# Kernel tuning notes

Hardware: AMD Instinct MI355X
Metric: run time of the kernel (lower is better)

The kernel has to match this reference:

```python
import jax, jax.numpy as jnp
import numpy as np

TOP_K = 2  # module default top_k


def setup_inputs() -> dict:
    key = jax.random.key(0)
    k1, k2, k3 = jax.random.split(key, 3)
    B, D, E = 4096, 1024, 64  # tokens, input_dim, num_experts
    return {
        "tensor1": jax.random.normal(k1, (B, D), dtype=jnp.float32),
        "tensor2": jax.random.normal(k2, (B, D), dtype=jnp.float32),
        "gate_weight": jax.random.normal(k3, (E, 2 * D), dtype=jnp.float32) * 0.02,
    }


def reference(tensor1, tensor2, gate_weight):
    # x: (B, 2D)
    x = jnp.concatenate((tensor1, tensor2), axis=-1)
    # pairwise L2 distance between each token and each expert vector
    diff = gate_weight[None, :, :] - x[:, None, :]          # (B, E, 2D)
    logits = -jnp.sqrt(jnp.sum(diff * diff, axis=-1))        # (B, E)
    topk_logits, indices = jax.lax.top_k(logits, TOP_K)      # (B, K)
    gating_weights = jax.nn.softmax(topk_logits, axis=-1)    # (B, K)
    rows = jnp.arange(logits.shape[0])[:, None]              # (B, 1)
    sparse_gating = jnp.zeros_like(logits).at[rows, indices].set(gating_weights)
    return sparse_gating
```

## Files before the change

kernel.cpp:

```cpp
#include <hip/hip_runtime.h>
#include <math.h>

#define NTOK 4096
#define NDIM 1024
#define KTOT 2048
#define NEXP 64
#define MT   64
#define KB   64
#define LSTR 72
#define NKC  8
#define NSTG 4

typedef _Float16 half8 __attribute__((ext_vector_type(8)));
typedef _Float16 half4 __attribute__((ext_vector_type(4)));
typedef float    floatx4 __attribute__((ext_vector_type(4)));

#define XSCALE 16.0f
#define WSCALE 1024.0f
#define INVSCALE (1.0f / (16.0f * 1024.0f))

struct h2pair { _Float16 h, l; };
__device__ __forceinline__ h2pair split2(float v) {
    h2pair r;
    r.h = (_Float16)v;
    r.l = (_Float16)(v - (float)r.h);
    return r;
}

__global__ __launch_bounds__(256) void prep_w(const float* __restrict__ W,
                                              _Float16* __restrict__ Whg,
                                              _Float16* __restrict__ Wlg,
                                              float* __restrict__ nrm) {
    const int e = blockIdx.x, t = threadIdx.x;
    const float* row = W + (size_t)e * KTOT + t * 8;
    const float4 a = *reinterpret_cast<const float4*>(row);
    const float4 b = *reinterpret_cast<const float4*>(row + 4);
    float ss = fmaf(a.x, a.x, fmaf(a.y, a.y, fmaf(a.z, a.z, fmaf(a.w, a.w, 0.f))));
    ss = fmaf(b.x, b.x, fmaf(b.y, b.y, fmaf(b.z, b.z, fmaf(b.w, b.w, ss))));

    const h2pair p0 = split2(a.x * WSCALE), p1 = split2(a.y * WSCALE);
    const h2pair p2 = split2(a.z * WSCALE), p3 = split2(a.w * WSCALE);
    const h2pair p4 = split2(b.x * WSCALE), p5 = split2(b.y * WSCALE);
    const h2pair p6 = split2(b.z * WSCALE), p7 = split2(b.w * WSCALE);
    half8 h, l;
    h[0]=p0.h; h[1]=p1.h; h[2]=p2.h; h[3]=p3.h; h[4]=p4.h; h[5]=p5.h; h[6]=p6.h; h[7]=p7.h;
    l[0]=p0.l; l[1]=p1.l; l[2]=p2.l; l[3]=p3.l; l[4]=p4.l; l[5]=p5.l; l[6]=p6.l; l[7]=p7.l;
    *reinterpret_cast<half8*>(Whg + (size_t)e * KTOT + t * 8) = h;
    *reinterpret_cast<half8*>(Wlg + (size_t)e * KTOT + t * 8) = l;

    #pragma unroll
    for (int off = 32; off > 0; off >>= 1) ss += __shfl_down(ss, off, 64);
    __shared__ float red[4];
    const int lane = t & 63, wv = t >> 6;
    if (lane == 0) red[wv] = ss;
    __syncthreads();
    if (t == 0) nrm[e] = (red[0] + red[1]) + (red[2] + red[3]);
}

__global__ __launch_bounds__(256, 3) void gemm_mfma(const float* __restrict__ t1,
                                                    const float* __restrict__ t2,
                                                    const _Float16* __restrict__ Whg,
                                                    const _Float16* __restrict__ Wlg,
                                                    float* __restrict__ Gp,
                                                    float* __restrict__ Cp) {
    __shared__ _Float16 Xh[MT * LSTR], Xl[MT * LSTR];
    __shared__ _Float16 Wh[NEXP * LSTR], Wl[NEXP * LSTR];

    const int tid  = threadIdx.x;
    const int lane = tid & 63;
    const int wv   = tid >> 6;
    const int srow = tid >> 4;
    const int scol = tid & 15;
    const int wrow = tid >> 2;
    const int wseg = tid & 3;
    const int kc   = blockIdx.y;
    const int kbase = kc * (NSTG * KB);
    const int tok0  = blockIdx.x * MT;

    const float* __restrict__ xsrc = (kbase < NDIM)
        ? (t1 + (size_t)tok0 * NDIM + kbase)
        : (t2 + (size_t)tok0 * NDIM + (kbase - NDIM));
    const _Float16* __restrict__ whsrc = Whg + (size_t)wrow * KTOT + kbase + wseg * 16;
    const _Float16* __restrict__ wlsrc = Wlg + (size_t)wrow * KTOT + kbase + wseg * 16;
    _Float16* whdst = Wh + wrow * LSTR + wseg * 16;
    _Float16* wldst = Wl + wrow * LSTR + wseg * 16;

    floatx4 acc[4];
    #pragma unroll
    for (int j = 0; j < 4; ++j) { acc[j][0] = 0.f; acc[j][1] = 0.f; acc[j][2] = 0.f; acc[j][3] = 0.f; }
    float ssx[4] = {0.f, 0.f, 0.f, 0.f};

    const int frow = lane & 15;
    const int fq   = lane >> 4;
    const _Float16* xh_p = Xh + (16 * wv + frow) * LSTR + fq * 8;
    const _Float16* xl_p = Xl + (16 * wv + frow) * LSTR + fq * 8;

    #pragma unroll
    for (int s = 0; s < NSTG; ++s) {
        {
            const half8 wh0 = *reinterpret_cast<const half8*>(whsrc + s * KB);
            const half8 wh1 = *reinterpret_cast<const half8*>(whsrc + s * KB + 8);
            const half8 wl0 = *reinterpret_cast<const half8*>(wlsrc + s * KB);
            const half8 wl1 = *reinterpret_cast<const half8*>(wlsrc + s * KB + 8);
            *reinterpret_cast<half8*>(whdst)     = wh0;
            *reinterpret_cast<half8*>(whdst + 8) = wh1;
            *reinterpret_cast<half8*>(wldst)     = wl0;
            *reinterpret_cast<half8*>(wldst + 8) = wl1;
        }
        #pragma unroll
        for (int i = 0; i < 4; ++i) {
            const int row = srow + 16 * i;
            const float4 xv = *reinterpret_cast<const float4*>(
                xsrc + (size_t)row * NDIM + s * KB + scol * 4);
            ssx[i] = fmaf(xv.x, xv.x, fmaf(xv.y, xv.y, fmaf(xv.z, xv.z, fmaf(xv.w, xv.w, ssx[i]))));
            const h2pair x0 = split2(xv.x * XSCALE), x1 = split2(xv.y * XSCALE);
            const h2pair x2 = split2(xv.z * XSCALE), x3 = split2(xv.w * XSCALE);
            half4 hx, lx;
            hx[0] = x0.h; hx[1] = x1.h; hx[2] = x2.h; hx[3] = x3.h;
            lx[0] = x0.l; lx[1] = x1.l; lx[2] = x2.l; lx[3] = x3.l;
            *reinterpret_cast<half4*>(Xh + row * LSTR + scol * 4) = hx;
            *reinterpret_cast<half4*>(Xl + row * LSTR + scol * 4) = lx;
        }
        __syncthreads();

        #pragma unroll
        for (int ks = 0; ks < 2; ++ks) {
            const int ko = ks * 32;
            const half8 ah = *reinterpret_cast<const half8*>(xh_p + ko);
            const half8 al = *reinterpret_cast<const half8*>(xl_p + ko);
            half8 bh[4], bl[4];
            #pragma unroll
            for (int j = 0; j < 4; ++j) {
                bh[j] = *reinterpret_cast<const half8*>(Wh + (16 * j + frow) * LSTR + fq * 8 + ko);
                bl[j] = *reinterpret_cast<const half8*>(Wl + (16 * j + frow) * LSTR + fq * 8 + ko);
            }
            #pragma unroll
            for (int j = 0; j < 4; ++j)
                acc[j] = __builtin_amdgcn_mfma_f32_16x16x32_f16(ah, bh[j], acc[j], 0, 0, 0);
            #pragma unroll
            for (int j = 0; j < 4; ++j)
                acc[j] = __builtin_amdgcn_mfma_f32_16x16x32_f16(al, bh[j], acc[j], 0, 0, 0);
            #pragma unroll
            for (int j = 0; j < 4; ++j)
                acc[j] = __builtin_amdgcn_mfma_f32_16x16x32_f16(ah, bl[j], acc[j], 0, 0, 0);
        }
        __syncthreads();
    }

    const int m0 = 16 * wv + fq * 4;
    #pragma unroll
    for (int j = 0; j < 4; ++j) {
        #pragma unroll
        for (int i = 0; i < 4; ++i) {
            Gp[((size_t)kc * NTOK + tok0 + m0 + i) * NEXP + 16 * j + frow] = acc[j][i];
        }
    }

    #pragma unroll
    for (int off = 1; off < 16; off <<= 1) {
        #pragma unroll
        for (int i = 0; i < 4; ++i) ssx[i] += __shfl_xor(ssx[i], off, 64);
    }
    if (scol == 0) {
        #pragma unroll
        for (int i = 0; i < 4; ++i)
            Cp[(size_t)kc * NTOK + tok0 + srow + 16 * i] = ssx[i];
    }
}

__global__ __launch_bounds__(256) void finalize(const float* __restrict__ Gp,
                                                const float* __restrict__ Cp,
                                                const float* __restrict__ nrm,
                                                float* __restrict__ out) {
    const int wv = threadIdx.x >> 6, lane = threadIdx.x & 63;
    const int token = blockIdx.x * 4 + wv;

    float gsum = 0.f, csum = 0.f;
    #pragma unroll
    for (int cix = 0; cix < NKC; ++cix) {
        gsum += Gp[((size_t)cix * NTOK + token) * NEXP + lane];
        csum += Cp[(size_t)cix * NTOK + token];
    }
    const float nv = nrm[lane];

    const float S = fmaf(-2.f * INVSCALE, gsum, csum) + nv;
    const float logit = -sqrtf(S);

    float v1 = logit; int i1 = lane;
    #pragma unroll
    for (int off = 32; off > 0; off >>= 1) {
        float ov = __shfl_xor(v1, off, 64);
        int   oi = __shfl_xor(i1, off, 64);
        if (ov > v1 || (ov == v1 && oi < i1)) { v1 = ov; i1 = oi; }
    }
    float v2 = (lane == i1) ? -__builtin_inff() : logit;
    int   i2 = lane;
    #pragma unroll
    for (int off = 32; off > 0; off >>= 1) {
        float ov = __shfl_xor(v2, off, 64);
        int   oi = __shfl_xor(i2, off, 64);
        if (ov > v2 || (ov == v2 && oi < i2)) { v2 = ov; i2 = oi; }
    }
    const float e2  = expf(v2 - v1);
    const float inv = 1.f / (1.f + e2);
    const float o = (lane == i1) ? inv : ((lane == i2) ? e2 * inv : 0.f);
    out[(size_t)token * NEXP + lane] = o;
}

extern "C" void kernel_launch(void* const* d_in, const int* in_sizes, int n_in,
                              void* d_out, int out_size, void* d_ws, size_t ws_size,
                              hipStream_t stream) {
    const float* t1 = (const float*)d_in[0];
    const float* t2 = (const float*)d_in[1];
    const float* W  = (const float*)d_in[2];
    float* out = (float*)d_out;

    char* ws = (char*)d_ws;
    float*    Gp  = (float*)ws;
    float*    Cp  = Gp + (size_t)NKC * NTOK * NEXP;
    float*    nrm = Cp + (size_t)NKC * NTOK;
    _Float16* Whg = (_Float16*)(nrm + NEXP);
    _Float16* Wlg = Whg + (size_t)NEXP * KTOT;

    prep_w<<<NEXP, 256, 0, stream>>>(W, Whg, Wlg, nrm);
    gemm_mfma<<<dim3(NTOK / MT, NKC), 256, 0, stream>>>(t1, t2, Whg, Wlg, Gp, Cp);
    finalize<<<NTOK / 4, 256, 0, stream>>>(Gp, Cp, nrm, out);
}
```

Measured before the change: 88.98 us.

## Drop LDS staging; load MFMA fragments directly from global with fragment-ordered weights

The weight hi/lo halves are now stored in a fragment-interleaved layout (k-group major, expert, 8 halves), so each lane can load its MFMA B operand straight from global memory. The GEMM kernel no longer stages X or W through shared memory and has no barriers. Each wave independently handles 16 tokens by one K chunk and converts X to hi/lo fp16 in registers. This removes LDS traffic and syncs, at the cost of each wave re-reading the weight slice from L2 instead of sharing it across a block, and of less latency hiding between loads and MFMAs.

Measured after the change: 89.96 us. No clear change (+1.1%).

```diff
diff --git a/kernel.cpp b/kernel.cpp
--- a/kernel.cpp
+++ b/kernel.cpp
@@ -5,14 +5,11 @@
 #define NDIM 1024
 #define KTOT 2048
 #define NEXP 64
-#define MT   64
-#define KB   64
-#define LSTR 72
 #define NKC  8
-#define NSTG 4
+#define KCH  (KTOT / NKC)
+#define NSTEP (KCH / 32)
 
 typedef _Float16 half8 __attribute__((ext_vector_type(8)));
-typedef _Float16 half4 __attribute__((ext_vector_type(4)));
 typedef float    floatx4 __attribute__((ext_vector_type(4)));
 
 #define XSCALE 16.0f
@@ -28,8 +25,8 @@
 }
 
 __global__ __launch_bounds__(256) void prep_w(const float* __restrict__ W,
-                                              _Float16* __restrict__ Whg,
-                                              _Float16* __restrict__ Wlg,
+                                              _Float16* __restrict__ WhT,
+                                              _Float16* __restrict__ WlT,
                                               float* __restrict__ nrm) {
     const int e = blockIdx.x, t = threadIdx.x;
     const float* row = W + (size_t)e * KTOT + t * 8;
@@ -45,8 +42,9 @@
     half8 h, l;
     h[0]=p0.h; h[1]=p1.h; h[2]=p2.h; h[3]=p3.h; h[4]=p4.h; h[5]=p5.h; h[6]=p6.h; h[7]=p7.h;
     l[0]=p0.l; l[1]=p1.l; l[2]=p2.l; l[3]=p3.l; l[4]=p4.l; l[5]=p5.l; l[6]=p6.l; l[7]=p7.l;
-    *reinterpret_cast<half8*>(Whg + (size_t)e * KTOT + t * 8) = h;
-    *reinterpret_cast<half8*>(Wlg + (size_t)e * KTOT + t * 8) = l;
+    const size_t idx = ((size_t)t * NEXP + e) * 8;
+    *reinterpret_cast<half8*>(WhT + idx) = h;
+    *reinterpret_cast<half8*>(WlT + idx) = l;
 
     #pragma unroll
     for (int off = 32; off > 0; off >>= 1) ss += __shfl_down(ss, off, 64);
@@ -57,115 +55,75 @@
     if (t == 0) nrm[e] = (red[0] + red[1]) + (red[2] + red[3]);
 }
 
-__global__ __launch_bounds__(256, 3) void gemm_mfma(const float* __restrict__ t1,
-                                                    const float* __restrict__ t2,
-                                                    const _Float16* __restrict__ Whg,
-                                                    const _Float16* __restrict__ Wlg,
-                                                    float* __restrict__ Gp,
-                                                    float* __restrict__ Cp) {
-    __shared__ _Float16 Xh[MT * LSTR], Xl[MT * LSTR];
-    __shared__ _Float16 Wh[NEXP * LSTR], Wl[NEXP * LSTR];
-
+__global__ __launch_bounds__(256) void gemm_frag(const float* __restrict__ t1,
+                                                 const float* __restrict__ t2,
+                                                 const _Float16* __restrict__ WhT,
+                                                 const _Float16* __restrict__ WlT,
+                                                 float* __restrict__ Gp,
+                                                 float* __restrict__ Cp) {
     const int tid  = threadIdx.x;
     const int lane = tid & 63;
-    const int wv   = tid >> 6;
-    const int srow = tid >> 4;
-    const int scol = tid & 15;
-    const int wrow = tid >> 2;
-    const int wseg = tid & 3;
-    const int kc   = blockIdx.y;
-    const int kbase = kc * (NSTG * KB);
-    const int tok0  = blockIdx.x * MT;
+    const int gw   = blockIdx.x * 4 + (tid >> 6);
+    const int tokg = gw >> 3;
+    const int kc   = gw & 7;
+    const int tok0 = tokg * 16;
+    const int kbase = kc * KCH;
+    const int n  = lane & 15;
+    const int fq = lane >> 4;
 
-    const float* __restrict__ xsrc = (kbase < NDIM)
-        ? (t1 + (size_t)tok0 * NDIM + kbase)
-        : (t2 + (size_t)tok0 * NDIM + (kbase - NDIM));
-    const _Float16* __restrict__ whsrc = Whg + (size_t)wrow * KTOT + kbase + wseg * 16;
-    const _Float16* __restrict__ wlsrc = Wlg + (size_t)wrow * KTOT + kbase + wseg * 16;
-    _Float16* whdst = Wh + wrow * LSTR + wseg * 16;
-    _Float16* wldst = Wl + wrow * LSTR + wseg * 16;
+    const float* __restrict__ xb = ((kbase < NDIM)
+        ? (t1 + (size_t)(tok0 + n) * NDIM + kbase)
+        : (t2 + (size_t)(tok0 + n) * NDIM + (kbase - NDIM))) + fq * 8;
+    const _Float16* __restrict__ whb = WhT + ((size_t)(kbase >> 3) + fq) * (NEXP * 8) + n * 8;
+    const _Float16* __restrict__ wlb = WlT + ((size_t)(kbase >> 3) + fq) * (NEXP * 8) + n * 8;
 
     floatx4 acc[4];
     #pragma unroll
-    for (int j = 0; j < 4; ++j) { acc[j][0] = 0.f; acc[j][1] = 0.f; acc[j][2] = 0.f; acc[j][3] = 0.f; }
-    float ssx[4] = {0.f, 0.f, 0.f, 0.f};
-
-    const int frow = lane & 15;
-    const int fq   = lane >> 4;
-    const _Float16* xh_p = Xh + (16 * wv + frow) * LSTR + fq * 8;
-    const _Float16* xl_p = Xl + (16 * wv + frow) * LSTR + fq * 8;
+    for (int j = 0; j < 4; ++j) { acc[j][0]=0.f; acc[j][1]=0.f; acc[j][2]=0.f; acc[j][3]=0.f; }
+    float ssx = 0.f;
 
     #pragma unroll
-    for (int s = 0; s < NSTG; ++s) {
-        {
-            const half8 wh0 = *reinterpret_cast<const half8*>(whsrc + s * KB);
-            const half8 wh1 = *reinterpret_cast<const half8*>(whsrc + s * KB + 8);
-            const half8 wl0 = *reinterpret_cast<const half8*>(wlsrc + s * KB);
-            const half8 wl1 = *reinterpret_cast<const half8*>(wlsrc + s * KB + 8);
-            *reinterpret_cast<half8*>(whdst)     = wh0;
-            *reinterpret_cast<half8*>(whdst + 8) = wh1;
-            *reinterpret_cast<half8*>(wldst)     = wl0;
-            *reinterpret_cast<half8*>(wldst + 8) = wl1;
+    for (int s = 0; s < NSTEP; ++s) {
+        const float4 x0 = *reinterpret_cast<const float4*>(xb + s * 32);
+        const float4 x1 = *reinterpret_cast<const float4*>(xb + s * 32 + 4);
+        half8 bh[4], bl[4];
+        #pragma unroll
+        for (int j = 0; j < 4; ++j) {
+            bh[j] = *reinterpret_cast<const half8*>(whb + (size_t)s * 4 * (NEXP * 8) + j * 128);
+            bl[j] = *reinterpret_cast<const half8*>(wlb + (size_t)s * 4 * (NEXP * 8) + j * 128);
         }
+        ssx = fmaf(x0.x, x0.x, fmaf(x0.y, x0.y, fmaf(x0.z, x0.z, fmaf(x0.w, x0.w, ssx))));
+        ssx = fmaf(x1.x, x1.x, fmaf(x1.y, x1.y, fmaf(x1.z, x1.z, fmaf(x1.w, x1.w, ssx))));
+        const h2pair q0 = split2(x0.x * XSCALE), q1 = split2(x0.y * XSCALE);
+        const h2pair q2 = split2(x0.z * XSCALE), q3 = split2(x0.w * XSCALE);
+        const h2pair q4 = split2(x1.x * XSCALE), q5 = split2(x1.y * XSCALE);
+        const h2pair q6 = split2(x1.z * XSCALE), q7 = split2(x1.w * XSCALE);
+        half8 ah, al;
+        ah[0]=q0.h; ah[1]=q1.h; ah[2]=q2.h; ah[3]=q3.h; ah[4]=q4.h; ah[5]=q5.h; ah[6]=q6.h; ah[7]=q7.h;
+        al[0]=q0.l; al[1]=q1.l; al[2]=q2.l; al[3]=q3.l; al[4]=q4.l; al[5]=q5.l; al[6]=q6.l; al[7]=q7.l;
         #pragma unroll
-        for (int i = 0; i < 4; ++i) {
-            const int row = srow + 16 * i;
-            const float4 xv = *reinterpret_cast<const float4*>(
-                xsrc + (size_t)row * NDIM + s * KB + scol * 4);
-            ssx[i] = fmaf(xv.x, xv.x, fmaf(xv.y, xv.y, fmaf(xv.z, xv.z, fmaf(xv.w, xv.w, ssx[i]))));
-            const h2pair x0 = split2(xv.x * XSCALE), x1 = split2(xv.y * XSCALE);
-            const h2pair x2 = split2(xv.z * XSCALE), x3 = split2(xv.w * XSCALE);
-            half4 hx, lx;
-            hx[0] = x0.h; hx[1] = x1.h; hx[2] = x2.h; hx[3] = x3.h;
-            lx[0] = x0.l; lx[1] = x1.l; lx[2] = x2.l; lx[3] = x3.l;
-            *reinterpret_cast<half4*>(Xh + row * LSTR + scol * 4) = hx;
-            *reinterpret_cast<half4*>(Xl + row * LSTR + scol * 4) = lx;
-        }
-        __syncthreads();
-
+        for (int j = 0; j < 4; ++j)
+            acc[j] = __builtin_amdgcn_mfma_f32_16x16x32_f16(ah, bh[j], acc[j], 0, 0, 0);
         #pragma unroll
-        for (int ks = 0; ks < 2; ++ks) {
-            const int ko = ks * 32;
-            const half8 ah = *reinterpret_cast<const half8*>(xh_p + ko);
-            const half8 al = *reinterpret_cast<const half8*>(xl_p + ko);
-            half8 bh[4], bl[4];
-            #pragma unroll
-            for (int j = 0; j < 4; ++j) {
-                bh[j] = *reinterpret_cast<const half8*>(Wh + (16 * j + frow) * LSTR + fq * 8 + ko);
-                bl[j] = *reinterpret_cast<const half8*>(Wl + (16 * j + frow) * LSTR + fq * 8 + ko);
-            }
-            #pragma unroll
-            for (int j = 0; j < 4; ++j)
-                acc[j] = __builtin_amdgcn_mfma_f32_16x16x32_f16(ah, bh[j], acc[j], 0, 0, 0);
-            #pragma unroll
-            for (int j = 0; j < 4; ++j)
-                acc[j] = __builtin_amdgcn_mfma_f32_16x16x32_f16(al, bh[j], acc[j], 0, 0, 0);
-            #pragma unroll
-            for (int j = 0; j < 4; ++j)
-                acc[j] = __builtin_amdgcn_mfma_f32_16x16x32_f16(ah, bl[j], acc[j], 0, 0, 0);
-        }
-        __syncthreads();
+        for (int j = 0; j < 4; ++j)
+            acc[j] = __builtin_amdgcn_mfma_f32_16x16x32_f16(al, bh[j], acc[j], 0, 0, 0);
+        #pragma unroll
+        for (int j = 0; j < 4; ++j)
+            acc[j] = __builtin_amdgcn_mfma_f32_16x16x32_f16(ah, bl[j], acc[j], 0, 0, 0);
     }
 
-    const int m0 = 16 * wv + fq * 4;
     #pragma unroll
     for (int j = 0; j < 4; ++j) {
         #pragma unroll
         for (int i = 0; i < 4; ++i) {
-            Gp[((size_t)kc * NTOK + tok0 + m0 + i) * NEXP + 16 * j + frow] = acc[j][i];
+            Gp[((size_t)kc * NTOK + tok0 + fq * 4 + i) * NEXP + 16 * j + n] = acc[j][i];
         }
     }
 
-    #pragma unroll
-    for (int off = 1; off < 16; off <<= 1) {
-        #pragma unroll
-        for (int i = 0; i < 4; ++i) ssx[i] += __shfl_xor(ssx[i], off, 64);
-    }
-    if (scol == 0) {
-        #pragma unroll
-        for (int i = 0; i < 4; ++i)
-            Cp[(size_t)kc * NTOK + tok0 + srow + 16 * i] = ssx[i];
-    }
+    ssx += __shfl_xor(ssx, 16, 64);
+    ssx += __shfl_xor(ssx, 32, 64);
+    if (lane < 16)
+        Cp[(size_t)kc * NTOK + tok0 + lane] = ssx;
 }
 
 __global__ __launch_bounds__(256) void finalize(const float* __restrict__ Gp,
@@ -219,10 +177,10 @@
     float*    Gp  = (float*)ws;
     float*    Cp  = Gp + (size_t)NKC * NTOK * NEXP;
     float*    nrm = Cp + (size_t)NKC * NTOK;
-    _Float16* Whg = (_Float16*)(nrm + NEXP);
-    _Float16* Wlg = Whg + (size_t)NEXP * KTOT;
+    _Float16* WhT = (_Float16*)(nrm + NEXP);
+    _Float16* WlT = WhT + (size_t)NEXP * KTOT;
 
-    prep_w<<<NEXP, 256, 0, stream>>>(W, Whg, Wlg, nrm);
-    gemm_mfma<<<dim3(NTOK / MT, NKC), 256, 0, stream>>>(t1, t2, Whg, Wlg, Gp, Cp);
+    prep_w<<<NEXP, 256, 0, stream>>>(W, WhT, WlT, nrm);
+    gemm_frag<<<(NTOK / 16) * NKC / 4, 256, 0, stream>>>(t1, t2, WhT, WlT, Gp, Cp);
     finalize<<<NTOK / 4, 256, 0, stream>>>(Gp, Cp, nrm, out);
 }
```
